# Performance work log

Measured on AMD Instinct MI355X. Metric: run time of the kernel, lower is better.

## Reference

```python
import jax, jax.numpy as jnp
import numpy as np

V, T, E, HID = 50000, 32, 256, 512
H = HID // 2  # per-direction LSTM hidden
L, B = 512, 64


def setup_inputs() -> dict:
    key = jax.random.key(0)
    ks = jax.random.split(key, 18)
    p = lambda k, shape: (jax.random.normal(k, shape, jnp.float32) * 0.1)
    return {
        'seqs': jax.random.randint(ks[0], (L, B), 0, V),
        'tags': jax.random.randint(ks[1], (L, B), 0, T),
        'masks': jnp.ones((L, B), jnp.int32),
        'embed_table': p(ks[2], (V, E)),
        'W_ih_f': p(ks[3], (4 * H, E)), 'W_hh_f': p(ks[4], (4 * H, H)),
        'b_ih_f': p(ks[5], (4 * H,)),   'b_hh_f': p(ks[6], (4 * H,)),
        'W_ih_b': p(ks[7], (4 * H, E)), 'W_hh_b': p(ks[8], (4 * H, H)),
        'b_ih_b': p(ks[9], (4 * H,)),   'b_hh_b': p(ks[10], (4 * H,)),
        'W_out': p(ks[11], (T, HID)),   'b_out': p(ks[12], (T,)),
        'start_trans': p(ks[13], (T,)), 'end_trans': p(ks[14], (T,)),
        'trans': p(ks[15], (T, T)),
    }


def _lstm(xs, mask_b, W_ih, W_hh, b_ih, b_hh, reverse):
    # xs: [L,B,E], mask_b: [L,B] bool. Masked updates emulate packed sequences
    # (state frozen and output zeroed at padded steps).
    Bsz = xs.shape[1]
    Hd = W_hh.shape[1]
    x_proj = jnp.einsum('lbe,ge->lbg', xs, W_ih) + b_ih + b_hh  # precompute input gates

    def step(carry, inp):
        h, c = carry
        xg, m = inp
        gates = xg + h @ W_hh.T
        i, f, g, o = jnp.split(gates, 4, axis=-1)  # torch gate order i,f,g,o
        i, f, o = jax.nn.sigmoid(i), jax.nn.sigmoid(f), jax.nn.sigmoid(o)
        g = jnp.tanh(g)
        c_new = f * c + i * g
        h_new = o * jnp.tanh(c_new)
        m = m[:, None]
        h = jnp.where(m, h_new, h)
        c = jnp.where(m, c_new, c)
        out = jnp.where(m, h_new, 0.0)
        return (h, c), out

    init = (jnp.zeros((Bsz, Hd), xs.dtype), jnp.zeros((Bsz, Hd), xs.dtype))
    _, outs = jax.lax.scan(step, init, (x_proj, mask_b), reverse=reverse)
    return outs  # [L,B,H]


def reference(seqs, tags, masks, embed_table,
              W_ih_f, W_hh_f, b_ih_f, b_hh_f,
              W_ih_b, W_hh_b, b_ih_b, b_hh_b,
              W_out, b_out, start_trans, end_trans, trans):
    mb = masks.astype(bool)  # [L,B]
    emb = embed_table[seqs]  # [L,B,E]; dropout is identity in eval mode
    h_f = _lstm(emb, mb, W_ih_f, W_hh_f, b_ih_f, b_hh_f, reverse=False)
    h_b = _lstm(emb, mb, W_ih_b, W_hh_b, b_ih_b, b_hh_b, reverse=True)
    lstm_out = jnp.concatenate([h_f, h_b], axis=-1)           # [L,B,HID]
    emissions = jnp.einsum('lbh,th->lbt', lstm_out, W_out) + b_out  # [L,B,T]

    Lb, Bb = seqs.shape
    mf = masks[1:].astype(emissions.dtype)  # [L-1,B]

    # ---- gold path score (pytorch-crf numerator) ----
    e_scores = jnp.take_along_axis(emissions, tags[:, :, None], axis=2)[:, :, 0]  # [L,B]
    t_scores = trans[tags[:-1], tags[1:]]                                         # [L-1,B]
    lengths = masks.sum(0)
    last_tags = tags[lengths - 1, jnp.arange(Bb)]
    numerator = (start_trans[tags[0]] + e_scores[0]
                 + ((e_scores[1:] + t_scores) * mf).sum(0)
                 + end_trans[last_tags])  # [B]

    # ---- partition function (forward algorithm) ----
    def part_step(score, xs):
        e_t, m_t = xs  # [B,T], [B]
        nxt = jax.nn.logsumexp(score[:, :, None] + trans[None] + e_t[:, None, :], axis=1)
        return jnp.where(m_t[:, None], nxt, score), None

    score0 = start_trans[None, :] + emissions[0]
    score, _ = jax.lax.scan(part_step, score0, (emissions[1:], mb[1:]))
    log_z = jax.nn.logsumexp(score + end_trans[None, :], axis=1)  # [B]

    llh = numerator - log_z
    return -llh.mean()
```

## Files before the change

kernel.cpp:

```cpp
#include <hip/hip_runtime.h>
#include <hip/hip_bf16.h>
#include <stdint.h>

#define DEVINL __device__ __forceinline__

typedef __attribute__((ext_vector_type(8))) short short8;
typedef __attribute__((ext_vector_type(4))) float float4v;
typedef __attribute__((ext_vector_type(4))) int int4v;

#define NLC (-1.4426950408889634f)

DEVINL float bf2f(short s) {
  union { unsigned u; float f; } v; v.u = ((unsigned)(unsigned short)s) << 16; return v.f;
}
DEVINL unsigned short f2bf(float f) {
  union { float f; unsigned u; } v; v.f = f;
  unsigned r = v.u + 0x7FFFu + ((v.u >> 16) & 1u);
  return (unsigned short)(r >> 16);
}
DEVINL unsigned cvt_pk_bf16(float lo, float hi) {
  unsigned r;
  asm("v_cvt_pk_bf16_f32 %0, %1, %2" : "=v"(r) : "v"(lo), "v"(hi));
  return r;
}
DEVINL float ex2(float x) { return __builtin_amdgcn_exp2f(x); }
DEVINL float rcp_(float x) { return __builtin_amdgcn_rcpf(x); }

__global__ void k_cvt(const float* __restrict__ src, short* __restrict__ dst, int n8) {
  int i = blockIdx.x * blockDim.x + threadIdx.x;
  int stride = gridDim.x * blockDim.x;
  for (; i < n8; i += stride) {
    const float4v* s = (const float4v*)(src + (size_t)i * 8);
    float4v a = s[0], b = s[1];
    short8 o;
    o[0] = (short)f2bf(a[0]); o[1] = (short)f2bf(a[1]);
    o[2] = (short)f2bf(a[2]); o[3] = (short)f2bf(a[3]);
    o[4] = (short)f2bf(b[0]); o[5] = (short)f2bf(b[1]);
    o[6] = (short)f2bf(b[2]); o[7] = (short)f2bf(b[3]);
    ((short8*)dst)[i] = o;
  }
}

__global__ void k_bias(const float* __restrict__ a1, const float* __restrict__ a2,
                       const float* __restrict__ b1, const float* __restrict__ b2,
                       float* __restrict__ o) {
  int i = blockIdx.x * blockDim.x + threadIdx.x;
  o[i] = (i < 1024) ? (a1[i] + a2[i]) : (b1[i - 1024] + b2[i - 1024]);
}

__global__ void k_wmax(const float* __restrict__ Wf, const float* __restrict__ Wb,
                       unsigned* __restrict__ wmax) {
  int i = blockIdx.x * blockDim.x + threadIdx.x;
  int stride = gridDim.x * blockDim.x;
  unsigned mf = 0, mb = 0;
  for (int k = i; k < 262144; k += stride) {
    mf = max(mf, __float_as_uint(fabsf(Wf[k])));
    mb = max(mb, __float_as_uint(fabsf(Wb[k])));
  }
#pragma unroll
  for (int o = 32; o > 0; o >>= 1) {
    mf = max(mf, (unsigned)__shfl_down((int)mf, o));
    mb = max(mb, (unsigned)__shfl_down((int)mb, o));
  }
  if ((threadIdx.x & 63) == 0) { atomicMax(wmax + 0, mf); atomicMax(wmax + 1, mb); }
}

__global__ void k_wquant(const float* __restrict__ Wf, const float* __restrict__ Wb,
                         const float* __restrict__ wmax, char* __restrict__ whhQ) {
  int idx = blockIdx.x * blockDim.x + threadIdx.x;
  int dir = idx >> 16;
  int rem = idx & 65535;
  int r = rem >> 6;
  int k = (rem & 63) * 4;
  const float* W = dir ? Wb : Wf;
  float s = 127.0f / fmaxf(wmax[dir], 1e-20f);
  int g = r >> 8, unit = r & 255;
  int w = unit >> 6, m = (unit >> 4) & 3, row = unit & 15;
  int kt = k >> 6, l4 = (k >> 4) & 3, j = k & 15;
  int lane = l4 * 16 + row;
  unsigned out = 0;
#pragma unroll
  for (int t = 0; t < 4; ++t) {
    float v = W[(size_t)r * 256 + k + t] * s;
    int q = (int)rintf(v);
    q = q < -127 ? -127 : (q > 127 ? 127 : q);
    out |= ((unsigned)(q & 255)) << (8 * t);
  }
  *(unsigned*)(whhQ + (size_t)dir * 262144 + g * 65536 + w * 16384 + m * 4096 + kt * 1024 + lane * 16 + j) = out;
}

__launch_bounds__(256)
__global__ void k_xproj(const int* __restrict__ seqs, const short* __restrict__ embT,
                        const short* __restrict__ wihX, const float* __restrict__ biasX,
                        short* __restrict__ xproj) {
  __shared__ short As[128 * 256];
  __shared__ short Bs[128 * 256];
  __shared__ int ids[128];
  const int bm = blockIdx.x >> 4, bn = blockIdx.x & 15;
  const int tid = threadIdx.x;
  if (tid < 128) ids[tid] = seqs[bm * 128 + tid];
  __syncthreads();
#pragma unroll
  for (int i = 0; i < 16; ++i) {
    int task = tid + i * 256, row = task >> 5, kc = task & 31;
    short8 v = *(const short8*)(embT + (size_t)ids[row] * 256 + kc * 8);
    *(short8*)((char*)As + row * 512 + ((kc * 16) ^ ((row & 7) << 4))) = v;
  }
#pragma unroll
  for (int i = 0; i < 16; ++i) {
    int task = tid + i * 256, row = task >> 5, kc = task & 31;
    short8 v = *(const short8*)(wihX + (size_t)(bn * 128 + row) * 256 + kc * 8);
    *(short8*)((char*)Bs + row * 512 + ((kc * 16) ^ ((row & 7) << 4))) = v;
  }
  __syncthreads();
  const int wave = tid >> 6, lane = tid & 63, l15 = lane & 15, l4 = lane >> 4;
  float4v acc[2][8];
#pragma unroll
  for (int m = 0; m < 2; ++m)
#pragma unroll
    for (int n = 0; n < 8; ++n) acc[m][n] = (float4v){0.f, 0.f, 0.f, 0.f};
#pragma unroll
  for (int kt = 0; kt < 8; ++kt) {
    const int kb = kt * 64 + l4 * 16;
    short8 a[2], b[8];
#pragma unroll
    for (int m = 0; m < 2; ++m) {
      int row = (wave * 2 + m) * 16 + l15;
      a[m] = *(short8*)((char*)As + row * 512 + (kb ^ ((row & 7) << 4)));
    }
#pragma unroll
    for (int n = 0; n < 8; ++n) {
      int row = n * 16 + l15;
      b[n] = *(short8*)((char*)Bs + row * 512 + (kb ^ ((row & 7) << 4)));
    }
#pragma unroll
    for (int m = 0; m < 2; ++m)
#pragma unroll
      for (int n = 0; n < 8; ++n)
        acc[m][n] = __builtin_amdgcn_mfma_f32_16x16x32_bf16(a[m], b[n], acc[m][n], 0, 0, 0);
  }
#pragma unroll
  for (int n = 0; n < 8; ++n) {
    int col = bn * 128 + n * 16 + l15;
    float bias = biasX[col];
    float scale = (((col >> 8) & 3) == 2) ? (2.f * NLC) : NLC;
#pragma unroll
    for (int m = 0; m < 2; ++m) {
      int token = bm * 128 + (wave * 2 + m) * 16 + l4 * 4;
#pragma unroll
      for (int q = 0; q < 4; ++q)
        xproj[(size_t)(token + q) * 2048 + col] = (short)f2bf((acc[m][n][q] + bias) * scale);
    }
  }
}

__launch_bounds__(512, 2)
__global__ void k_lstm(const short* __restrict__ xproj, const char* __restrict__ whhQ,
                       const float* __restrict__ wmax, const int* __restrict__ masks,
                       short* __restrict__ h_all) {
  __shared__ char lds_h[2][16 * 256];
  const int bid = blockIdx.x;
  const int dir = bid & 1, bq = bid >> 1;
  const int tid = threadIdx.x, w = tid >> 6, lane = tid & 63;
  const int beta = lane & 15, l4 = lane >> 4;
  const int bglob = bq * 16 + beta;
  const float wm = wmax[dir] * (1.0f / 16129.0f);
  const float facS = wm * NLC;
  const float facG = wm * 2.f * NLC;

  int4v wf[4][2][4];
  {
    const char* base = whhQ + (size_t)dir * 262144 + lane * 16;
#pragma unroll
    for (int g = 0; g < 4; ++g)
#pragma unroll
      for (int m = 0; m < 2; ++m) {
        int t = w * 2 + m;
#pragma unroll
        for (int kt = 0; kt < 4; ++kt)
          wf[g][m][kt] = *(const int4v*)(base + g * 65536 + (t >> 2) * 16384 + (t & 3) * 4096 + kt * 1024);
      }
  }

  int rd_off[4], wr_off[2];
#pragma unroll
  for (int kt = 0; kt < 4; ++kt)
    rd_off[kt] = beta * 256 + ((kt * 64 + l4 * 16) ^ ((beta & 7) << 4));
#pragma unroll
  for (int m = 0; m < 2; ++m)
    wr_off[m] = beta * 256 + ((w * 32 + m * 16 + l4 * 4) ^ ((beta & 7) << 4));

  if (tid < 256) ((int4v*)lds_h[0])[tid] = (int4v){0, 0, 0, 0};

  float c[2][4], hq[2][4];
#pragma unroll
  for (int m = 0; m < 2; ++m)
#pragma unroll
    for (int q = 0; q < 4; ++q) { c[m][q] = 0.f; hq[m][q] = 0.f; }

  const short* xb = xproj + dir * 1024 + w * 32 + l4 * 4;
  union XPU { unsigned long long u; short s[4]; };
  XPU xp[4][2], xpn[4][2];
  {
    int t0 = dir ? 511 : 0;
#pragma unroll
    for (int g = 0; g < 4; ++g)
#pragma unroll
      for (int m = 0; m < 2; ++m)
        xp[g][m].u = *(const unsigned long long*)(xb + (size_t)(t0 * 64 + bglob) * 2048 + g * 256 + m * 16);
  }
  int mcur = masks[(dir ? 511 : 0) * 64 + bglob];

  auto SUBSTEP = [&](int step, const char* rb, char* wb) {
    const int tseq = dir ? (511 - step) : step;
    asm volatile("s_waitcnt lgkmcnt(0)" ::: "memory");
    __builtin_amdgcn_sched_barrier(0);
    __builtin_amdgcn_s_barrier();
    __builtin_amdgcn_sched_barrier(0);
    int4v bfr[4];
#pragma unroll
    for (int kt = 0; kt < 4; ++kt) bfr[kt] = *(const int4v*)(rb + rd_off[kt]);

    int ns = step + 1 < 512 ? step + 1 : 511;
    int tn = dir ? (511 - ns) : ns;
    const short* xa = xb + (size_t)(tn * 64 + bglob) * 2048;
#pragma unroll
    for (int g = 0; g < 4; ++g)
#pragma unroll
      for (int m = 0; m < 2; ++m)
        xpn[g][m].u = *(const unsigned long long*)(xa + g * 256 + m * 16);
    int mn = masks[tn * 64 + bglob];

    int4v iacc[4][2];
#pragma unroll
    for (int g = 0; g < 4; ++g)
#pragma unroll
      for (int m = 0; m < 2; ++m) {
        int4v t = __builtin_amdgcn_mfma_i32_16x16x64_i8(wf[g][m][0], bfr[0], (int4v){0, 0, 0, 0}, 0, 0, 0);
        t = __builtin_amdgcn_mfma_i32_16x16x64_i8(wf[g][m][1], bfr[1], t, 0, 0, 0);
        t = __builtin_amdgcn_mfma_i32_16x16x64_i8(wf[g][m][2], bfr[2], t, 0, 0, 0);
        iacc[g][m] = __builtin_amdgcn_mfma_i32_16x16x64_i8(wf[g][m][3], bfr[3], t, 0, 0, 0);
      }

    size_t hoff = (size_t)(tseq * 64 + bglob) * 512 + dir * 256 + w * 32 + l4 * 4;
#pragma unroll
    for (int m = 0; m < 2; ++m) {
      int qi[4];
      float ov_[4];
#pragma unroll
      for (int q = 0; q < 4; ++q) {
        float ai = fmaf((float)iacc[0][m][q], facS, bf2f(xp[0][m].s[q]));
        float af = fmaf((float)iacc[1][m][q], facS, bf2f(xp[1][m].s[q]));
        float ag = fmaf((float)iacc[2][m][q], facG, bf2f(xp[2][m].s[q]));
        float ao = fmaf((float)iacc[3][m][q], facS, bf2f(xp[3][m].s[q]));
        float iv = rcp_(1.f + ex2(ai));
        float fv = rcp_(1.f + ex2(af));
        float gv = fmaf(2.f, rcp_(1.f + ex2(ag)), -1.f);
        float ovv = rcp_(1.f + ex2(ao));
        float cn = fmaf(fv, c[m][q], iv * gv);
        float tc = fmaf(2.f, rcp_(1.f + ex2(cn * (2.f * NLC))), -1.f);
        float hn = ovv * tc;
        c[m][q] = mcur ? cn : c[m][q];
        float hv = mcur ? hn : hq[m][q];
        hq[m][q] = hv;
        ov_[q] = mcur ? hn : 0.f;
        qi[q] = (int)rintf(hv * 127.f);
      }
      unsigned p0 = __builtin_amdgcn_perm((unsigned)qi[1], (unsigned)qi[0], 0x0c0c0400u);
      unsigned p1 = __builtin_amdgcn_perm((unsigned)qi[3], (unsigned)qi[2], 0x0c0c0400u);
      unsigned qpack = __builtin_amdgcn_perm(p1, p0, 0x05040100u);
      *(unsigned*)(wb + wr_off[m]) = qpack;
      uint2 ob;
      ob.x = cvt_pk_bf16(ov_[0], ov_[1]);
      ob.y = cvt_pk_bf16(ov_[2], ov_[3]);
      *(uint2*)(h_all + hoff + m * 16) = ob;
    }
#pragma unroll
    for (int g = 0; g < 4; ++g)
#pragma unroll
      for (int m = 0; m < 2; ++m) xp[g][m] = xpn[g][m];
    mcur = mn;
  };

#pragma unroll 1
  for (int s2 = 0; s2 < 256; ++s2) {
    SUBSTEP(2 * s2,     lds_h[0], lds_h[1]);
    SUBSTEP(2 * s2 + 1, lds_h[1], lds_h[0]);
  }
}

__launch_bounds__(256)
__global__ void k_emis(const short* __restrict__ h_all, const short* __restrict__ woutX,
                       const float* __restrict__ bout, float* __restrict__ emis) {
  const int tid = threadIdx.x, wave = tid >> 6, lane = tid & 63;
  const int l15 = lane & 15, l4 = lane >> 4;
  const int token0 = blockIdx.x * 256 + wave * 64;
  float4v acc[4][2];
#pragma unroll
  for (int m = 0; m < 4; ++m)
#pragma unroll
    for (int n = 0; n < 2; ++n) acc[m][n] = (float4v){0.f, 0.f, 0.f, 0.f};
#pragma unroll
  for (int kt = 0; kt < 16; ++kt) {
    short8 b[2];
#pragma unroll
    for (int n = 0; n < 2; ++n)
      b[n] = *(const short8*)(woutX + (size_t)(n * 16 + l15) * 512 + kt * 32 + l4 * 8);
#pragma unroll
    for (int m = 0; m < 4; ++m) {
      short8 a = *(const short8*)(h_all + (size_t)(token0 + m * 16 + l15) * 512 + kt * 32 + l4 * 8);
#pragma unroll
      for (int n = 0; n < 2; ++n)
        acc[m][n] = __builtin_amdgcn_mfma_f32_16x16x32_bf16(a, b[n], acc[m][n], 0, 0, 0);
    }
  }
#pragma unroll
  for (int n = 0; n < 2; ++n) {
    float bias = bout[n * 16 + l15];
#pragma unroll
    for (int m = 0; m < 4; ++m) {
      int token = token0 + m * 16 + l4 * 4;
#pragma unroll
      for (int q = 0; q < 4; ++q)
        emis[(size_t)(token + q) * 32 + n * 16 + l15] = acc[m][n][q] + bias;
    }
  }
}

__launch_bounds__(64)
__global__ void k_crf(const float* __restrict__ emis, const int* __restrict__ tags,
                      const int* __restrict__ masks, const float* __restrict__ strans,
                      const float* __restrict__ etrans, const float* __restrict__ trans,
                      float* __restrict__ out) {
  __shared__ float trans_s[1024];
  __shared__ float score_s[32];
  const float L2E = 1.4426950408889634f;
  const int b = blockIdx.x, lane = threadIdx.x;
  for (int i = lane; i < 1024; i += 64) trans_s[i] = trans[i];

  float num = 0.f; int lensum = 0;
#pragma unroll 1
  for (int i = 0; i < 8; ++i) {
    int t = lane + i * 64;
    int tg = tags[t * 64 + b];
    int m = masks[t * 64 + b];
    lensum += m;
    float e = emis[(size_t)(t * 64 + b) * 32 + tg];
    if (t == 0) num += strans[tg] + e;
    else if (m) num += e + trans[tags[(t - 1) * 64 + b] * 32 + tg];
  }
#pragma unroll
  for (int o = 32; o > 0; o >>= 1) { num += __shfl_down(num, o); lensum += __shfl_down(lensum, o); }
  num = __shfl(num, 0);
  lensum = __shfl(lensum, 0);
  num += etrans[tags[(lensum - 1) * 64 + b]];
  __syncthreads();

  const int jp = lane & 31, half = lane >> 5;
  if (lane < 32) score_s[jp] = strans[jp] + emis[(size_t)b * 32 + jp];
  __syncthreads();

  float e_next = emis[(size_t)(64 + b) * 32 + jp];
#pragma unroll 1
  for (int t = 1; t < 512; ++t) {
    float e = e_next;
    if (t < 511) e_next = emis[(size_t)((t + 1) * 64 + b) * 32 + jp];
    int m = masks[t * 64 + b];
    float v[16], mx = -1e30f;
#pragma unroll
    for (int j = 0; j < 16; ++j) {
      v[j] = score_s[half * 16 + j] + trans_s[(half * 16 + j) * 32 + jp];
      mx = fmaxf(mx, v[j]);
    }
    float sum = 0.f;
#pragma unroll
    for (int j = 0; j < 16; ++j) sum += ex2((v[j] - mx) * L2E);
    float mo = __shfl_xor(mx, 32), so = __shfl_xor(sum, 32);
    float mn2 = fmaxf(mx, mo);
    sum = sum * ex2((mx - mn2) * L2E) + so * ex2((mo - mn2) * L2E);
    float nxt = e + mn2 + __builtin_amdgcn_logf(sum) * (1.f / L2E);
    float cur = score_s[jp];
    float ns = m ? nxt : cur;
    __syncthreads();
    if (lane < 32) score_s[jp] = ns;
    __syncthreads();
  }

  float vv = (lane < 32) ? (score_s[jp] + etrans[jp]) : -1e30f;
  float mx = vv;
#pragma unroll
  for (int o = 32; o > 0; o >>= 1) mx = fmaxf(mx, __shfl_xor(mx, o));
  float sm = (lane < 32) ? ex2((vv - mx) * L2E) : 0.f;
#pragma unroll
  for (int o = 32; o > 0; o >>= 1) sm += __shfl_xor(sm, o);
  float lz = mx + __builtin_amdgcn_logf(sm) * (1.f / L2E);
  if (lane == 0) atomicAdd(out, -(num - lz) * (1.0f / 64.0f));
}

extern "C" void kernel_launch(void* const* d_in, const int* in_sizes, int n_in,
                              void* d_out, int out_size, void* d_ws, size_t ws_size,
                              hipStream_t stream) {
  const int*   seqs  = (const int*)d_in[0];
  const int*   tags  = (const int*)d_in[1];
  const int*   masks = (const int*)d_in[2];
  const float* embed = (const float*)d_in[3];
  const float* Wihf  = (const float*)d_in[4];
  const float* Whhf  = (const float*)d_in[5];
  const float* bihf  = (const float*)d_in[6];
  const float* bhhf  = (const float*)d_in[7];
  const float* Wihb  = (const float*)d_in[8];
  const float* Whhb  = (const float*)d_in[9];
  const float* bihb  = (const float*)d_in[10];
  const float* bhhb  = (const float*)d_in[11];
  const float* Wout  = (const float*)d_in[12];
  const float* bout  = (const float*)d_in[13];
  const float* strn  = (const float*)d_in[14];
  const float* etrn  = (const float*)d_in[15];
  const float* trn   = (const float*)d_in[16];
  float* outf = (float*)d_out;

  char* ws = (char*)d_ws;
  short* xproj = (short*)(ws + 0);
  short* h_all = (short*)(ws + 134217728);
  float* emis  = (float*)(ws + 167772160);
  short* embT  = (short*)(ws + 171966464);
  short* wihX  = (short*)(ws + 197566464);
  char*  whhQ  = (char*)(ws + 198615040);
  unsigned* wmaxb = (unsigned*)(ws + 199139328);
  short* woutX = (short*)(ws + 199663616);
  float* biasX = (float*)(ws + 199696384);

  hipMemsetAsync(d_out, 0, 4, stream);
  hipMemsetAsync(wmaxb, 0, 8, stream);

  k_cvt<<<2048, 256, 0, stream>>>(embed, embT, 1600000);
  k_cvt<<<128, 256, 0, stream>>>(Wihf, wihX, 32768);
  k_cvt<<<128, 256, 0, stream>>>(Wihb, wihX + 262144, 32768);
  k_cvt<<<8, 256, 0, stream>>>(Wout, woutX, 2048);
  k_bias<<<2, 1024, 0, stream>>>(bihf, bhhf, bihb, bhhb, biasX);
  k_wmax<<<64, 256, 0, stream>>>(Whhf, Whhb, wmaxb);
  k_wquant<<<512, 256, 0, stream>>>(Whhf, Whhb, (const float*)wmaxb, whhQ);
  k_xproj<<<4096, 256, 0, stream>>>(seqs, embT, wihX, biasX, xproj);
  k_lstm<<<8, 512, 0, stream>>>(xproj, whhQ, (const float*)wmaxb, masks, h_all);
  k_emis<<<128, 256, 0, stream>>>(h_all, woutX, bout, emis);
  k_crf<<<64, 64, 0, stream>>>(emis, tags, masks, strn, etrn, trn, outf);
}
```

Before: 1.611 ms.

## Reuse gathered embeddings across N tiles and streamline LSTM step math

The input-projection kernel now launches one block per 128-token tile. The gathered embedding A-tile stays in registers while the block loops over all 16 weight column tiles, so embeddings are no longer re-gathered once per N tile. The LSTM recurrence swaps index recomputation for pointer increments and double-buffers the next-step inputs through ping-pong register arrays. It also merges sigmoid and tanh reciprocals into shared divisions, using clamped exponentials, and quantises h with a magic-number add instead of rintf. Masks are copied into the workspace first. The cost is far fewer blocks for the projection GEMM, which lowers parallelism, plus slightly different numerics from the merged reciprocals.

```diff
diff --git a/kernel.cpp b/kernel.cpp
--- a/kernel.cpp
+++ b/kernel.cpp
@@ -10,9 +10,8 @@
 
 #define NLC (-1.4426950408889634f)
 
-DEVINL float bf2f(short s) {
-  union { unsigned u; float f; } v; v.u = ((unsigned)(unsigned short)s) << 16; return v.f;
-}
+DEVINL float uif(unsigned u) { union { unsigned u; float f; } v; v.u = u; return v.f; }
+DEVINL float bf2f(short s) { return uif(((unsigned)(unsigned short)s) << 16); }
 DEVINL unsigned short f2bf(float f) {
   union { float f; unsigned u; } v; v.f = f;
   unsigned r = v.u + 0x7FFFu + ((v.u >> 16) & 1u);
@@ -25,6 +24,18 @@
 }
 DEVINL float ex2(float x) { return __builtin_amdgcn_exp2f(x); }
 DEVINL float rcp_(float x) { return __builtin_amdgcn_rcpf(x); }
+DEVINL void unp4(unsigned long long u, float* f) {
+  unsigned lo = (unsigned)u, hi = (unsigned)(u >> 32);
+  f[0] = uif(lo << 16); f[1] = uif(lo & 0xffff0000u);
+  f[2] = uif(hi << 16); f[3] = uif(hi & 0xffff0000u);
+}
+
+#define LBAR() do { \
+  asm volatile("s_waitcnt lgkmcnt(0)" ::: "memory"); \
+  __builtin_amdgcn_sched_barrier(0); \
+  __builtin_amdgcn_s_barrier(); \
+  __builtin_amdgcn_sched_barrier(0); \
+} while (0)
 
 __global__ void k_cvt(const float* __restrict__ src, short* __restrict__ dst, int n8) {
   int i = blockIdx.x * blockDim.x + threadIdx.x;
@@ -96,7 +107,7 @@
   __shared__ short As[128 * 256];
   __shared__ short Bs[128 * 256];
   __shared__ int ids[128];
-  const int bm = blockIdx.x >> 4, bn = blockIdx.x & 15;
+  const int bm = blockIdx.x;
   const int tid = threadIdx.x;
   if (tid < 128) ids[tid] = seqs[bm * 128 + tid];
   __syncthreads();
@@ -106,57 +117,65 @@
     short8 v = *(const short8*)(embT + (size_t)ids[row] * 256 + kc * 8);
     *(short8*)((char*)As + row * 512 + ((kc * 16) ^ ((row & 7) << 4))) = v;
   }
-#pragma unroll
-  for (int i = 0; i < 16; ++i) {
-    int task = tid + i * 256, row = task >> 5, kc = task & 31;
-    short8 v = *(const short8*)(wihX + (size_t)(bn * 128 + row) * 256 + kc * 8);
-    *(short8*)((char*)Bs + row * 512 + ((kc * 16) ^ ((row & 7) << 4))) = v;
-  }
   __syncthreads();
   const int wave = tid >> 6, lane = tid & 63, l15 = lane & 15, l4 = lane >> 4;
-  float4v acc[2][8];
-#pragma unroll
-  for (int m = 0; m < 2; ++m)
-#pragma unroll
-    for (int n = 0; n < 8; ++n) acc[m][n] = (float4v){0.f, 0.f, 0.f, 0.f};
-#pragma unroll
-  for (int kt = 0; kt < 8; ++kt) {
-    const int kb = kt * 64 + l4 * 16;
-    short8 a[2], b[8];
-#pragma unroll
-    for (int m = 0; m < 2; ++m) {
-      int row = (wave * 2 + m) * 16 + l15;
-      a[m] = *(short8*)((char*)As + row * 512 + (kb ^ ((row & 7) << 4)));
+  short8 af[2][8];
+#pragma unroll
+  for (int m = 0; m < 2; ++m) {
+    int row = (wave * 2 + m) * 16 + l15;
+#pragma unroll
+    for (int kt = 0; kt < 8; ++kt)
+      af[m][kt] = *(short8*)((char*)As + row * 512 + ((kt * 64 + l4 * 16) ^ ((row & 7) << 4)));
+  }
+#pragma unroll 1
+  for (int bn = 0; bn < 16; ++bn) {
+    __syncthreads();
+#pragma unroll
+    for (int i = 0; i < 16; ++i) {
+      int task = tid + i * 256, row = task >> 5, kc = task & 31;
+      short8 v = *(const short8*)(wihX + (size_t)(bn * 128 + row) * 256 + kc * 8);
+      *(short8*)((char*)Bs + row * 512 + ((kc * 16) ^ ((row & 7) << 4))) = v;
+    }
+    __syncthreads();
+    float4v acc[2][8];
+#pragma unroll
+    for (int m = 0; m < 2; ++m)
+#pragma unroll
+      for (int n = 0; n < 8; ++n) acc[m][n] = (float4v){0.f, 0.f, 0.f, 0.f};
+#pragma unroll
+    for (int kt = 0; kt < 8; ++kt) {
+      const int kb = kt * 64 + l4 * 16;
+      short8 b[8];
+#pragma unroll
+      for (int n = 0; n < 8; ++n) {
+        int row = n * 16 + l15;
+        b[n] = *(short8*)((char*)Bs + row * 512 + (kb ^ ((row & 7) << 4)));
+      }
+#pragma unroll
+      for (int m = 0; m < 2; ++m)
+#pragma unroll
+        for (int n = 0; n < 8; ++n)
+          acc[m][n] = __builtin_amdgcn_mfma_f32_16x16x32_bf16(af[m][kt], b[n], acc[m][n], 0, 0, 0);
     }
 #pragma unroll
     for (int n = 0; n < 8; ++n) {
-      int row = n * 16 + l15;
-      b[n] = *(short8*)((char*)Bs + row * 512 + (kb ^ ((row & 7) << 4)));
-    }
-#pragma unroll
-    for (int m = 0; m < 2; ++m)
-#pragma unroll
-      for (int n = 0; n < 8; ++n)
-        acc[m][n] = __builtin_amdgcn_mfma_f32_16x16x32_bf16(a[m], b[n], acc[m][n], 0, 0, 0);
-  }
-#pragma unroll
-  for (int n = 0; n < 8; ++n) {
-    int col = bn * 128 + n * 16 + l15;
-    float bias = biasX[col];
-    float scale = (((col >> 8) & 3) == 2) ? (2.f * NLC) : NLC;
-#pragma unroll
-    for (int m = 0; m < 2; ++m) {
-      int token = bm * 128 + (wave * 2 + m) * 16 + l4 * 4;
-#pragma unroll
-      for (int q = 0; q < 4; ++q)
-        xproj[(size_t)(token + q) * 2048 + col] = (short)f2bf((acc[m][n][q] + bias) * scale);
+      int col = bn * 128 + n * 16 + l15;
+      float bias = biasX[col];
+      float scale = (((col >> 8) & 3) == 2) ? (2.f * NLC) : NLC;
+#pragma unroll
+      for (int m = 0; m < 2; ++m) {
+        int token = bm * 128 + (wave * 2 + m) * 16 + l4 * 4;
+#pragma unroll
+        for (int q = 0; q < 4; ++q)
+          xproj[(size_t)(token + q) * 2048 + col] = (short)f2bf((acc[m][n][q] + bias) * scale);
+      }
     }
   }
 }
 
 __launch_bounds__(512, 2)
 __global__ void k_lstm(const short* __restrict__ xproj, const char* __restrict__ whhQ,
-                       const float* __restrict__ wmax, const int* __restrict__ masks,
+                       const float* __restrict__ wmax, const int* __restrict__ mask_ws,
                        short* __restrict__ h_all) {
   __shared__ char lds_h[2][16 * 256];
   const int bid = blockIdx.x;
@@ -198,38 +217,39 @@
 #pragma unroll
     for (int q = 0; q < 4; ++q) { c[m][q] = 0.f; hq[m][q] = 0.f; }
 
-  const short* xb = xproj + dir * 1024 + w * 32 + l4 * 4;
-  union XPU { unsigned long long u; short s[4]; };
-  XPU xp[4][2], xpn[4][2];
-  {
-    int t0 = dir ? 511 : 0;
+  const int t0 = dir ? 511 : 0;
+  const int SD = dir ? -131072 : 131072;
+  const int SM = dir ? -64 : 64;
+  const int SH = dir ? -32768 : 32768;
+  const short* px = xproj + (size_t)(t0 * 64 + bglob) * 2048 + dir * 1024 + w * 32 + l4 * 4;
+  const int* pm = mask_ws + t0 * 64 + bglob;
+  short* ph = h_all + (size_t)(t0 * 64 + bglob) * 512 + dir * 256 + w * 32 + l4 * 4;
+
+  unsigned long long X0[4][2], X1[4][2];
+  int m0, m1;
+#pragma unroll
+  for (int g = 0; g < 4; ++g)
+#pragma unroll
+    for (int m = 0; m < 2; ++m)
+      X0[g][m] = *(const unsigned long long*)(px + g * 256 + m * 16);
+  m0 = *pm;
+  px += SD; pm += SM;
+
+  auto SUB = [&](unsigned long long (&xc)[4][2], int& mc,
+                 unsigned long long (&xn)[4][2], int& mn,
+                 const char* rb, char* wb) {
+    LBAR();
+    int4v bfr[4];
+#pragma unroll
+    for (int kt = 0; kt < 4; ++kt) bfr[kt] = *(const int4v*)(rb + rd_off[kt]);
+
 #pragma unroll
     for (int g = 0; g < 4; ++g)
 #pragma unroll
       for (int m = 0; m < 2; ++m)
-        xp[g][m].u = *(const unsigned long long*)(xb + (size_t)(t0 * 64 + bglob) * 2048 + g * 256 + m * 16);
-  }
-  int mcur = masks[(dir ? 511 : 0) * 64 + bglob];
-
-  auto SUBSTEP = [&](int step, const char* rb, char* wb) {
-    const int tseq = dir ? (511 - step) : step;
-    asm volatile("s_waitcnt lgkmcnt(0)" ::: "memory");
-    __builtin_amdgcn_sched_barrier(0);
-    __builtin_amdgcn_s_barrier();
-    __builtin_amdgcn_sched_barrier(0);
-    int4v bfr[4];
-#pragma unroll
-    for (int kt = 0; kt < 4; ++kt) bfr[kt] = *(const int4v*)(rb + rd_off[kt]);
-
-    int ns = step + 1 < 512 ? step + 1 : 511;
-    int tn = dir ? (511 - ns) : ns;
-    const short* xa = xb + (size_t)(tn * 64 + bglob) * 2048;
-#pragma unroll
-    for (int g = 0; g < 4; ++g)
-#pragma unroll
-      for (int m = 0; m < 2; ++m)
-        xpn[g][m].u = *(const unsigned long long*)(xa + g * 256 + m * 16);
-    int mn = masks[tn * 64 + bglob];
+        xn[g][m] = *(const unsigned long long*)(px + g * 256 + m * 16);
+    mn = *pm;
+    px += SD; pm += SM;
 
     int4v iacc[4][2];
 #pragma unroll
@@ -242,50 +262,48 @@
         iacc[g][m] = __builtin_amdgcn_mfma_i32_16x16x64_i8(wf[g][m][3], bfr[3], t, 0, 0, 0);
       }
 
-    size_t hoff = (size_t)(tseq * 64 + bglob) * 512 + dir * 256 + w * 32 + l4 * 4;
 #pragma unroll
     for (int m = 0; m < 2; ++m) {
-      int qi[4];
-      float ov_[4];
+      float xi[4], xf[4], xg[4], xo[4];
+      unp4(xc[0][m], xi); unp4(xc[1][m], xf); unp4(xc[2][m], xg); unp4(xc[3][m], xo);
+      unsigned qb[4]; float ov[4];
 #pragma unroll
       for (int q = 0; q < 4; ++q) {
-        float ai = fmaf((float)iacc[0][m][q], facS, bf2f(xp[0][m].s[q]));
-        float af = fmaf((float)iacc[1][m][q], facS, bf2f(xp[1][m].s[q]));
-        float ag = fmaf((float)iacc[2][m][q], facG, bf2f(xp[2][m].s[q]));
-        float ao = fmaf((float)iacc[3][m][q], facS, bf2f(xp[3][m].s[q]));
-        float iv = rcp_(1.f + ex2(ai));
-        float fv = rcp_(1.f + ex2(af));
-        float gv = fmaf(2.f, rcp_(1.f + ex2(ag)), -1.f);
-        float ovv = rcp_(1.f + ex2(ao));
-        float cn = fmaf(fv, c[m][q], iv * gv);
-        float tc = fmaf(2.f, rcp_(1.f + ex2(cn * (2.f * NLC))), -1.f);
-        float hn = ovv * tc;
-        c[m][q] = mcur ? cn : c[m][q];
-        float hv = mcur ? hn : hq[m][q];
+        float ai = fmaf((float)iacc[0][m][q], facS, xi[q]);
+        float af_ = fmaf((float)iacc[1][m][q], facS, xf[q]);
+        float ag = fmaf((float)iacc[2][m][q], facG, xg[q]);
+        float ao = fmaf((float)iacc[3][m][q], facS, xo[q]);
+        float Ei = fminf(ex2(ai), 1e30f);
+        float Ef = fminf(ex2(af_), 1e30f);
+        float Eg = fminf(ex2(ag), 1e30f);
+        float Eo = fminf(ex2(ao), 1e30f);
+        float ig = (1.f - Eg) * rcp_((1.f + Ei) * (1.f + Eg));
+        float fv = rcp_(1.f + Ef);
+        float cn = fmaf(fv, c[m][q], ig);
+        float Ec = fminf(ex2(cn * (2.f * NLC)), 1e30f);
+        float hn = (1.f - Ec) * rcp_((1.f + Eo) * (1.f + Ec));
+        c[m][q] = mc ? cn : c[m][q];
+        float hv = mc ? hn : hq[m][q];
         hq[m][q] = hv;
-        ov_[q] = mcur ? hn : 0.f;
-        qi[q] = (int)rintf(hv * 127.f);
+        ov[q] = mc ? hn : 0.f;
+        qb[q] = __float_as_uint(fmaf(hv, 127.f, 12582912.f));
       }
-      unsigned p0 = __builtin_amdgcn_perm((unsigned)qi[1], (unsigned)qi[0], 0x0c0c0400u);
-      unsigned p1 = __builtin_amdgcn_perm((unsigned)qi[3], (unsigned)qi[2], 0x0c0c0400u);
+      unsigned p0 = __builtin_amdgcn_perm(qb[1], qb[0], 0x0c0c0400u);
+      unsigned p1 = __builtin_amdgcn_perm(qb[3], qb[2], 0x0c0c0400u);
       unsigned qpack = __builtin_amdgcn_perm(p1, p0, 0x05040100u);
       *(unsigned*)(wb + wr_off[m]) = qpack;
       uint2 ob;
-      ob.x = cvt_pk_bf16(ov_[0], ov_[1]);
-      ob.y = cvt_pk_bf16(ov_[2], ov_[3]);
-      *(uint2*)(h_all + hoff + m * 16) = ob;
-    }
-#pragma unroll
-    for (int g = 0; g < 4; ++g)
-#pragma unroll
-      for (int m = 0; m < 2; ++m) xp[g][m] = xpn[g][m];
-    mcur = mn;
+      ob.x = cvt_pk_bf16(ov[0], ov[1]);
+      ob.y = cvt_pk_bf16(ov[2], ov[3]);
+      *(uint2*)(ph + m * 16) = ob;
+    }
+    ph += SH;
   };
 
 #pragma unroll 1
   for (int s2 = 0; s2 < 256; ++s2) {
-    SUBSTEP(2 * s2,     lds_h[0], lds_h[1]);
-    SUBSTEP(2 * s2 + 1, lds_h[1], lds_h[0]);
+    SUB(X0, m0, X1, m1, lds_h[0], lds_h[1]);
+    SUB(X1, m1, X0, m0, lds_h[1], lds_h[0]);
   }
 }
 
@@ -420,18 +438,20 @@
   float* outf = (float*)d_out;
 
   char* ws = (char*)d_ws;
-  short* xproj = (short*)(ws + 0);
-  short* h_all = (short*)(ws + 134217728);
-  float* emis  = (float*)(ws + 167772160);
-  short* embT  = (short*)(ws + 171966464);
-  short* wihX  = (short*)(ws + 197566464);
-  char*  whhQ  = (char*)(ws + 198615040);
-  unsigned* wmaxb = (unsigned*)(ws + 199139328);
-  short* woutX = (short*)(ws + 199663616);
-  float* biasX = (float*)(ws + 199696384);
+  short* xproj = (short*)(ws + 262144);
+  short* h_all = (short*)(ws + 134479872);
+  float* emis  = (float*)(ws + 168034304);
+  short* embT  = (short*)(ws + 172228608);
+  short* wihX  = (short*)(ws + 197828608);
+  char*  whhQ  = (char*)(ws + 198877184);
+  short* woutX = (short*)(ws + 199401472);
+  float* biasX = (float*)(ws + 199434240);
+  unsigned* wmaxb = (unsigned*)(ws + 199442432);
+  int* mask_ws = (int*)(ws + 199442944);
 
   hipMemsetAsync(d_out, 0, 4, stream);
   hipMemsetAsync(wmaxb, 0, 8, stream);
+  hipMemcpyAsync(mask_ws, masks, 131072, hipMemcpyDeviceToDevice, stream);
 
   k_cvt<<<2048, 256, 0, stream>>>(embed, embT, 1600000);
   k_cvt<<<128, 256, 0, stream>>>(Wihf, wihX, 32768);
@@ -440,8 +460,8 @@
   k_bias<<<2, 1024, 0, stream>>>(bihf, bhhf, bihb, bhhb, biasX);
   k_wmax<<<64, 256, 0, stream>>>(Whhf, Whhb, wmaxb);
   k_wquant<<<512, 256, 0, stream>>>(Whhf, Whhb, (const float*)wmaxb, whhQ);
-  k_xproj<<<4096, 256, 0, stream>>>(seqs, embT, wihX, biasX, xproj);
-  k_lstm<<<8, 512, 0, stream>>>(xproj, whhQ, (const float*)wmaxb, masks, h_all);
+  k_xproj<<<256, 256, 0, stream>>>(seqs, embT, wihX, biasX, xproj);
+  k_lstm<<<8, 512, 0, stream>>>(xproj, whhQ, (const float*)wmaxb, mask_ws, h_all);
   k_emis<<<128, 256, 0, stream>>>(h_all, woutX, bout, emis);
   k_crf<<<64, 64, 0, stream>>>(emis, tags, masks, strn, etrn, trn, outf);
 }
```

Measured after the change: 1.590 ms. No clear change (-1.3%).
